# Performance work log

Hardware: AMD Instinct MI355X
Metric: run time of the kernel (lower is better)

The kernel has to match this reference:

```python
import jax, jax.numpy as jnp
import numpy as np

REFRACTORY_PERIOD = 5
DAMPENING_FACTOR = 0.3


def setup_inputs() -> dict:
    key = jax.random.key(0)
    B, T, N = 32, 4096, 256
    x = jax.random.normal(key, (B, T, N), dtype=jnp.float32)
    return {"x": x}


def _refractory_scan(x):
    # x: [B, T, N]; scan over time keeping refractory counter q resident.
    B, T, N = x.shape
    xt = jnp.swapaxes(x, 0, 1)  # [T, B, N]

    def step(q, x_t):
        cond = (x_t > 0) & (q == 0)
        z_t = jnp.where(cond, jnp.ones_like(q), jnp.zeros_like(q))
        q = jnp.maximum(jnp.zeros_like(q), q - 1) + REFRACTORY_PERIOD * z_t
        return q, z_t

    q0 = jnp.zeros((B, N), dtype=x.dtype)
    # Note: the t=0 case in the original (z0 = x0>0, q = R*z0) is exactly the
    # first step of this scan starting from q0 = 0.
    _, z = jax.lax.scan(step, q0, xt)
    return jnp.swapaxes(z, 0, 1)  # [B, T, N]


def reference(x) -> jnp.ndarray:
    # Forward value is exactly z_forward (the surrogate-gradient straight-through
    # construction leaves the value unchanged).
    return _refractory_scan(x)
```

## Files before the change

kernel.cpp:

```cpp
#include <hip/hip_runtime.h>
#include <cstdint>
#include <cstddef>

#define BB 32
#define TT 4096
#define NN 256
#define NNV 64
#define CC 128
#define PSUB 4
#define PP 32
#define PG 8

__global__ __launch_bounds__(256) void refrac_scan(const float* __restrict__ x,
                                                   uint32_t* __restrict__ tbl,
                                                   uint32_t* __restrict__ bits_g) {
    const int tid = threadIdx.x;
    const int pg = blockIdx.x >> 5;
    const int b  = blockIdx.x & 31;
    const int psub = tid >> 6;
    const int n4 = tid & 63;
    const int p = pg * PSUB + psub;

    const float4* __restrict__ xv = reinterpret_cast<const float4*>(x)
        + ((size_t)b * TT + (size_t)p * CC) * NNV + n4;

    int na[4][6];
    #pragma unroll
    for (int c = 0; c < 4; ++c)
        #pragma unroll
        for (int e = 0; e < 6; ++e) na[c][e] = e;

    uint32_t bits[4][4];

    #pragma unroll
    for (int w = 0; w < 4; ++w) {
        uint32_t cur[4] = {0u, 0u, 0u, 0u};
        for (int jb = 0; jb < 32; jb += 8) {
            float4 buf[8];
            #pragma unroll
            for (int u = 0; u < 8; ++u)
                buf[u] = xv[(size_t)(w * 32 + jb + u) * NNV];
            #pragma unroll
            for (int u = 0; u < 8; ++u) {
                const int j2 = jb + u;
                const int j  = w * 32 + j2;
                const float4 v = buf[u];
                const float fv[4] = {v.x, v.y, v.z, v.w};
                #pragma unroll
                for (int c = 0; c < 4; ++c) {
                    const bool pos = fv[c] > 0.0f;
                    cur[c] |= pos ? (1u << j2) : 0u;
                    #pragma unroll
                    for (int e = 0; e < 6; ++e)
                        if (pos & (j >= na[c][e])) na[c][e] = j + 6;
                }
            }
        }
        #pragma unroll
        for (int c = 0; c < 4; ++c) bits[c][w] = cur[c];
    }

    const size_t row = (size_t)b * PP + p;

    uint32_t t4[4];
    #pragma unroll
    for (int c = 0; c < 4; ++c) {
        uint32_t t = 0;
        #pragma unroll
        for (int e = 0; e < 6; ++e) {
            int q = na[c][e] - CC;
            q = q > 0 ? q : 0;
            t |= (uint32_t)q << (4 * e);
        }
        t4[c] = t;
    }
    reinterpret_cast<uint4*>(tbl)[row * NNV + n4] =
        make_uint4(t4[0], t4[1], t4[2], t4[3]);

    #pragma unroll
    for (int w = 0; w < 4; ++w)
        reinterpret_cast<uint4*>(bits_g)[(row * 4 + w) * NNV + n4] =
            make_uint4(bits[0][w], bits[1][w], bits[2][w], bits[3][w]);
}

__global__ __launch_bounds__(256) void refrac_emit(const uint32_t* __restrict__ tbl,
                                                   const uint32_t* __restrict__ bits_g,
                                                   float* __restrict__ z) {
    const int tid = threadIdx.x;
    const int pg = blockIdx.x >> 5;
    const int b  = blockIdx.x & 31;
    const int psub = tid >> 6;
    const int n4 = tid & 63;
    const int p = pg * PSUB + psub;
    const int pbase = pg * PSUB;

    __shared__ uint8_t ent_lds[PSUB][NN];

    {
        const int n = tid;
        uint32_t tv[PP];
        #pragma unroll
        for (int p2 = 0; p2 < PP; ++p2)
            tv[p2] = (p2 < pbase + PSUB - 1)
                         ? tbl[((size_t)b * PP + p2) * NN + n] : 0u;
        int e = 0;
        #pragma unroll
        for (int p2 = 0; p2 < PP; ++p2) {
            if (p2 >= pbase && p2 < pbase + PSUB)
                ent_lds[p2 - pbase][n] = (uint8_t)e;
            e = (int)((tv[p2] >> (4 * e)) & 0xFu);
        }
    }
    __syncthreads();

    const size_t row = (size_t)b * PP + p;
    uint32_t bw[4][4];
    #pragma unroll
    for (int w = 0; w < 4; ++w) {
        const uint4 bv =
            reinterpret_cast<const uint4*>(bits_g)[(row * 4 + w) * NNV + n4];
        bw[w][0] = bv.x; bw[w][1] = bv.y; bw[w][2] = bv.z; bw[w][3] = bv.w;
    }

    int ea[4];
    #pragma unroll
    for (int c = 0; c < 4; ++c) ea[c] = (int)ent_lds[psub][n4 * 4 + c];

    float4* __restrict__ zv = reinterpret_cast<float4*>(z)
        + ((size_t)b * TT + (size_t)p * CC) * NNV + n4;

    #pragma unroll
    for (int w = 0; w < 4; ++w) {
        for (int j2 = 0; j2 < 32; ++j2) {
            const int j = w * 32 + j2;
            float o[4];
            #pragma unroll
            for (int c = 0; c < 4; ++c) {
                const bool sp = (((bw[w][c] >> j2) & 1u) != 0u) & (j >= ea[c]);
                if (sp) ea[c] = j + 6;
                o[c] = sp ? 1.0f : 0.0f;
            }
            zv[(size_t)j * NNV] = make_float4(o[0], o[1], o[2], o[3]);
        }
    }
}

extern "C" void kernel_launch(void* const* d_in, const int* in_sizes, int n_in,
                              void* d_out, int out_size, void* d_ws, size_t ws_size,
                              hipStream_t stream) {
    const float* x = (const float*)d_in[0];
    float* z = (float*)d_out;

    uint32_t* tbl = (uint32_t*)d_ws;
    uint32_t* bits_g = (uint32_t*)((char*)d_ws + (size_t)BB * PP * NN * sizeof(uint32_t));

    refrac_scan<<<dim3(BB * PG), 256, 0, stream>>>(x, tbl, bits_g);
    refrac_emit<<<dim3(BB * PG), 256, 0, stream>>>(tbl, bits_g, z);
}
```

Measured before the change: 250.9 us.

## Shrink chunks to 32 steps and add separate compose kernel for entry states

```diff
diff --git a/kernel.cpp b/kernel.cpp
--- a/kernel.cpp
+++ b/kernel.cpp
@@ -6,14 +6,14 @@
 #define TT 4096
 #define NN 256
 #define NNV 64
-#define CC 128
+#define CC 32
 #define PSUB 4
-#define PP 32
-#define PG 8
+#define PP 128
+#define PG 32
 
-__global__ __launch_bounds__(256) void refrac_scan(const float* __restrict__ x,
-                                                   uint32_t* __restrict__ tbl,
-                                                   uint32_t* __restrict__ bits_g) {
+__global__ __launch_bounds__(256, 4) void refrac_scan(const float* __restrict__ x,
+                                                      uint32_t* __restrict__ tbl,
+                                                      uint32_t* __restrict__ bits_g) {
     const int tid = threadIdx.x;
     const int pg = blockIdx.x >> 5;
     const int b  = blockIdx.x & 31;
@@ -30,34 +30,28 @@
         #pragma unroll
         for (int e = 0; e < 6; ++e) na[c][e] = e;
 
-    uint32_t bits[4][4];
+    uint32_t cur[4] = {0u, 0u, 0u, 0u};
 
     #pragma unroll
-    for (int w = 0; w < 4; ++w) {
-        uint32_t cur[4] = {0u, 0u, 0u, 0u};
-        for (int jb = 0; jb < 32; jb += 8) {
-            float4 buf[8];
+    for (int jb = 0; jb < CC; jb += 8) {
+        float4 buf[8];
+        #pragma unroll
+        for (int u = 0; u < 8; ++u)
+            buf[u] = xv[(size_t)(jb + u) * NNV];
+        #pragma unroll
+        for (int u = 0; u < 8; ++u) {
+            const int j = jb + u;
+            const float4 v = buf[u];
+            const float fv[4] = {v.x, v.y, v.z, v.w};
             #pragma unroll
-            for (int u = 0; u < 8; ++u)
-                buf[u] = xv[(size_t)(w * 32 + jb + u) * NNV];
-            #pragma unroll
-            for (int u = 0; u < 8; ++u) {
-                const int j2 = jb + u;
-                const int j  = w * 32 + j2;
-                const float4 v = buf[u];
-                const float fv[4] = {v.x, v.y, v.z, v.w};
+            for (int c = 0; c < 4; ++c) {
+                const bool pos = fv[c] > 0.0f;
+                cur[c] |= pos ? (1u << j) : 0u;
                 #pragma unroll
-                for (int c = 0; c < 4; ++c) {
-                    const bool pos = fv[c] > 0.0f;
-                    cur[c] |= pos ? (1u << j2) : 0u;
-                    #pragma unroll
-                    for (int e = 0; e < 6; ++e)
-                        if (pos & (j >= na[c][e])) na[c][e] = j + 6;
-                }
+                for (int e = 0; e < 6; ++e)
+                    if (pos & (j >= na[c][e])) na[c][e] = j + 6;
             }
         }
-        #pragma unroll
-        for (int c = 0; c < 4; ++c) bits[c][w] = cur[c];
     }
 
     const size_t row = (size_t)b * PP + p;
@@ -76,72 +70,62 @@
     }
     reinterpret_cast<uint4*>(tbl)[row * NNV + n4] =
         make_uint4(t4[0], t4[1], t4[2], t4[3]);
-
-    #pragma unroll
-    for (int w = 0; w < 4; ++w)
-        reinterpret_cast<uint4*>(bits_g)[(row * 4 + w) * NNV + n4] =
-            make_uint4(bits[0][w], bits[1][w], bits[2][w], bits[3][w]);
+    reinterpret_cast<uint4*>(bits_g)[row * NNV + n4] =
+        make_uint4(cur[0], cur[1], cur[2], cur[3]);
 }
 
-__global__ __launch_bounds__(256) void refrac_emit(const uint32_t* __restrict__ tbl,
-                                                   const uint32_t* __restrict__ bits_g,
-                                                   float* __restrict__ z) {
+__global__ __launch_bounds__(256) void refrac_compose(const uint32_t* __restrict__ tbl,
+                                                      uint8_t* __restrict__ entry) {
+    const int n = threadIdx.x;
+    const int b = blockIdx.x;
+    int e = 0;
+    for (int pb = 0; pb < PP; pb += 16) {
+        uint32_t tv[16];
+        #pragma unroll
+        for (int i = 0; i < 16; ++i)
+            tv[i] = tbl[((size_t)b * PP + pb + i) * NN + n];
+        #pragma unroll
+        for (int i = 0; i < 16; ++i) {
+            entry[((size_t)b * PP + pb + i) * NN + n] = (uint8_t)e;
+            e = (int)((tv[i] >> (4 * e)) & 0xFu);
+        }
+    }
+}
+
+__global__ __launch_bounds__(256, 4) void refrac_emit(const uint32_t* __restrict__ bits_g,
+                                                      const uint8_t* __restrict__ entry,
+                                                      float* __restrict__ z) {
     const int tid = threadIdx.x;
     const int pg = blockIdx.x >> 5;
     const int b  = blockIdx.x & 31;
     const int psub = tid >> 6;
     const int n4 = tid & 63;
     const int p = pg * PSUB + psub;
-    const int pbase = pg * PSUB;
-
-    __shared__ uint8_t ent_lds[PSUB][NN];
-
-    {
-        const int n = tid;
-        uint32_t tv[PP];
-        #pragma unroll
-        for (int p2 = 0; p2 < PP; ++p2)
-            tv[p2] = (p2 < pbase + PSUB - 1)
-                         ? tbl[((size_t)b * PP + p2) * NN + n] : 0u;
-        int e = 0;
-        #pragma unroll
-        for (int p2 = 0; p2 < PP; ++p2) {
-            if (p2 >= pbase && p2 < pbase + PSUB)
-                ent_lds[p2 - pbase][n] = (uint8_t)e;
-            e = (int)((tv[p2] >> (4 * e)) & 0xFu);
-        }
-    }
-    __syncthreads();
 
     const size_t row = (size_t)b * PP + p;
-    uint32_t bw[4][4];
-    #pragma unroll
-    for (int w = 0; w < 4; ++w) {
-        const uint4 bv =
-            reinterpret_cast<const uint4*>(bits_g)[(row * 4 + w) * NNV + n4];
-        bw[w][0] = bv.x; bw[w][1] = bv.y; bw[w][2] = bv.z; bw[w][3] = bv.w;
-    }
 
+    const uint32_t ew =
+        reinterpret_cast<const uint32_t*>(entry)[row * NNV + n4];
     int ea[4];
     #pragma unroll
-    for (int c = 0; c < 4; ++c) ea[c] = (int)ent_lds[psub][n4 * 4 + c];
+    for (int c = 0; c < 4; ++c) ea[c] = (int)((ew >> (8 * c)) & 0xFFu);
+
+    const uint4 bv = reinterpret_cast<const uint4*>(bits_g)[row * NNV + n4];
+    const uint32_t bw[4] = {bv.x, bv.y, bv.z, bv.w};
 
     float4* __restrict__ zv = reinterpret_cast<float4*>(z)
         + ((size_t)b * TT + (size_t)p * CC) * NNV + n4;
 
     #pragma unroll
-    for (int w = 0; w < 4; ++w) {
-        for (int j2 = 0; j2 < 32; ++j2) {
-            const int j = w * 32 + j2;
-            float o[4];
-            #pragma unroll
-            for (int c = 0; c < 4; ++c) {
-                const bool sp = (((bw[w][c] >> j2) & 1u) != 0u) & (j >= ea[c]);
-                if (sp) ea[c] = j + 6;
-                o[c] = sp ? 1.0f : 0.0f;
-            }
-            zv[(size_t)j * NNV] = make_float4(o[0], o[1], o[2], o[3]);
+    for (int j = 0; j < CC; ++j) {
+        float o[4];
+        #pragma unroll
+        for (int c = 0; c < 4; ++c) {
+            const bool sp = (((bw[c] >> j) & 1u) != 0u) & (j >= ea[c]);
+            if (sp) ea[c] = j + 6;
+            o[c] = sp ? 1.0f : 0.0f;
         }
+        zv[(size_t)j * NNV] = make_float4(o[0], o[1], o[2], o[3]);
     }
 }
 
@@ -152,8 +136,10 @@
     float* z = (float*)d_out;
 
     uint32_t* tbl = (uint32_t*)d_ws;
-    uint32_t* bits_g = (uint32_t*)((char*)d_ws + (size_t)BB * PP * NN * sizeof(uint32_t));
+    uint32_t* bits_g = (uint32_t*)((char*)d_ws + (size_t)BB * PP * NN * 4);
+    uint8_t*  entry  = (uint8_t*)((char*)d_ws + (size_t)BB * PP * NN * 8);
 
     refrac_scan<<<dim3(BB * PG), 256, 0, stream>>>(x, tbl, bits_g);
-    refrac_emit<<<dim3(BB * PG), 256, 0, stream>>>(tbl, bits_g, z);
+    refrac_compose<<<dim3(BB), 256, 0, stream>>>(tbl, entry);
+    refrac_emit<<<dim3(BB * PG), 256, 0, stream>>>(bits_g, entry, z);
 }
```

New measurement: 269.9 us. 1.08x slower.
